# Optimization experiments

Measured on AMD Instinct MI355X. Metric: run time of the kernel, lower is better.

Reference implementation:

```python
import jax, jax.numpy as jnp
import numpy as np

B, S, DIM = 2, 2048, 2048
H, KVH, HD = 16, 4, 128
WINDOW = 1024
SCALE = HD ** -0.5


def setup_inputs() -> dict:
    key = jax.random.key(0)
    ks = jax.random.split(key, 8)
    x = jax.random.normal(ks[0], (B, S, DIM), dtype=jnp.float32)
    # rotary tables (seqlen, head_dim//2)
    inv_freq = 1.0 / (10000.0 ** (jnp.arange(0, HD // 2, dtype=jnp.float32) / (HD // 2)))
    t = jnp.arange(S, dtype=jnp.float32)
    freqs = jnp.outer(t, inv_freq)
    cos = jnp.cos(freqs)
    sin = jnp.sin(freqs)
    positions = jnp.arange(S, dtype=jnp.int64) if jax.config.jax_enable_x64 else jnp.arange(S, dtype=jnp.int32)
    # causal sliding-window mask (S, S): allowed iff q-WINDOW < k <= q
    q_idx = jnp.arange(S)[:, None]
    k_idx = jnp.arange(S)[None, :]
    allowed = (k_idx <= q_idx) & (k_idx > q_idx - WINDOW)
    mask = jnp.where(allowed, 0.0, -1e9).astype(jnp.float32)
    wq = jax.random.normal(ks[1], (DIM, H * HD), dtype=jnp.float32) * (DIM ** -0.5)
    wk = jax.random.normal(ks[2], (DIM, KVH * HD), dtype=jnp.float32) * (DIM ** -0.5)
    wv = jax.random.normal(ks[3], (DIM, KVH * HD), dtype=jnp.float32) * (DIM ** -0.5)
    wo = jax.random.normal(ks[4], (H * HD, DIM), dtype=jnp.float32) * ((H * HD) ** -0.5)
    return {"x": x, "cos": cos, "sin": sin, "positions": positions, "mask": mask,
            "wq": wq, "wk": wk, "wv": wv, "wo": wo}


def _rope(q, k, cos, sin):
    # q,k: (B,S,heads,HD); cos,sin: (S, HD//2)
    half = q.shape[-1] // 2
    qr, qi = q[..., :half], q[..., half:]
    kr, ki = k[..., :half], k[..., half:]
    c = cos[None, :, None, :]
    s = sin[None, :, None, :]
    qc, qs = qr * c, qr * s
    kc, ks_ = kr * c, kr * s
    # faithful to source: out has 1.5*HD features (rotated real half + raw imag half)
    q_out = jnp.concatenate([qc - qs, qc + qs, qi], axis=-1)
    k_out = jnp.concatenate([kc - ks_, kc + ks_, ki], axis=-1)
    return q_out, k_out


def reference(x, cos, sin, positions, mask, wq, wk, wv, wo):
    b, s, _ = x.shape
    xq = (x @ wq).reshape(b, s, H, HD)
    xk = (x @ wk).reshape(b, s, KVH, HD)
    xv = (x @ wv).reshape(b, s, KVH, HD)
    xq, xk = _rope(xq, xk, cos, sin)  # (b,s,H,1.5*HD), (b,s,KVH,1.5*HD)
    repeats = H // KVH
    key = jnp.repeat(xk, repeats, axis=2)   # (b,s,H,1.5*HD)
    value = jnp.repeat(xv, repeats, axis=2)  # (b,s,H,HD)
    scores = jnp.einsum('bqhe,bkhe->bhqk', xq, key) * SCALE
    scores = scores + mask[None, None, :, :]
    probs = jax.nn.softmax(scores.astype(jnp.float32), axis=-1).astype(xq.dtype)
    out = jnp.einsum('bhqk,bkhd->bqhd', probs, value)
    out = out.reshape(b, s, H * HD)
    return out @ wo
```

## Files before the change

kernel.cpp:

```cpp
#include <hip/hip_runtime.h>


typedef __attribute__((ext_vector_type(4))) float f32x4;
typedef __attribute__((ext_vector_type(8))) short s16x8;
typedef __attribute__((ext_vector_type(4))) unsigned short u16x4;

#define DEV static __device__ __forceinline__

DEV unsigned short f2bf(float f) {
  unsigned int u = __float_as_uint(f);
  u += 0x7fffu + ((u >> 16) & 1u);
  return (unsigned short)(u >> 16);
}
DEV float bf2f(unsigned short us) {
  return __uint_as_float(((unsigned int)us) << 16);
}
DEV f32x4 mfma_bf16(s16x8 a, s16x8 b, f32x4 c) {
  return __builtin_amdgcn_mfma_f32_16x16x32_bf16(a, b, c, 0, 0, 0);
}

__global__ void k_sentinel(float* __restrict__ out, int n) {
  int i = blockIdx.x * blockDim.x + threadIdx.x;
  const int stride = gridDim.x * blockDim.x;
  for (; i < n; i += stride) out[i] = 1.0e6f;
}

__global__ void k_cvt_x(const float* __restrict__ x, unsigned short* __restrict__ xb, int n4) {
  int i = blockIdx.x * blockDim.x + threadIdx.x;
  const int stride = gridDim.x * blockDim.x;
  for (; i < n4; i += stride) {
    float4 v = ((const float4*)x)[i];
    u16x4 o = {f2bf(v.x), f2bf(v.y), f2bf(v.z), f2bf(v.w)};
    ((u16x4*)xb)[i] = o;
  }
}

__global__ void k_cvt_w(const float* __restrict__ w, unsigned short* __restrict__ wt,
                        int N, int qscale) {
  __shared__ unsigned short tile[64][66];
  const int n0 = blockIdx.x * 64, k0 = blockIdx.y * 64;
  const int t = threadIdx.x;
  const float SC = 0.08838834764831845f;
#pragma unroll
  for (int i = 0; i < 16; ++i) {
    const int idx = i * 256 + t;
    const int r = idx >> 6, c = idx & 63;
    float v = w[(k0 + r) * N + n0 + c];
    if (qscale) v *= ((((n0 + c) & 127) < 64) ? 2.f * SC : SC);
    tile[r][c] = f2bf(v);
  }
  __syncthreads();
#pragma unroll
  for (int i = 0; i < 16; ++i) {
    const int idx = i * 256 + t;
    const int rn = idx >> 6, ck = idx & 63;
    wt[(n0 + rn) * 2048 + k0 + ck] = tile[ck][rn];
  }
}

__global__ __launch_bounds__(256) void k_gemm(
    const unsigned short* __restrict__ A, const unsigned short* __restrict__ B,
    const int mode, unsigned short* __restrict__ Qo, unsigned short* __restrict__ Kp,
    unsigned short* __restrict__ Vo, float* __restrict__ Co,
    const float* __restrict__ cosp, const float* __restrict__ sinp) {
  __shared__ __align__(16) unsigned short As[4096];
  __shared__ __align__(16) unsigned short Bs[4096];
  char* As_c = (char*)As;
  char* Bs_c = (char*)Bs;
  const int t = threadIdx.x;
  const int lane = t & 63, wid = t >> 6;
  const int l16 = lane & 15, g = lane >> 4;
  const int wr = wid >> 1, wc = wid & 1;
  const int m0 = blockIdx.x * 128, n0 = blockIdx.y * 128;

  const unsigned short* pa = A + (m0 + (t >> 2)) * 2048 + ((t & 3) << 3);
  const unsigned short* pb = B + (n0 + (t >> 2)) * 2048 + ((t & 3) << 3);
  char* la = As_c + t * 16;
  char* lb = Bs_c + t * 16;

  f32x4 acc[4][4] = {};

  for (int kt = 0; kt < 64; ++kt) {
    const unsigned short* pak = pa + kt * 32;
    const unsigned short* pbk = pb + kt * 32;
    s16x8 a0 = *(const s16x8*)(pak);
    s16x8 a1 = *(const s16x8*)(pak + 64 * 2048);
    s16x8 b0 = *(const s16x8*)(pbk);
    s16x8 b1 = *(const s16x8*)(pbk + 64 * 2048);
    __syncthreads();
    *(s16x8*)la = a0;
    *(s16x8*)(la + 4096) = a1;
    *(s16x8*)lb = b0;
    *(s16x8*)(lb + 4096) = b1;
    __syncthreads();
    s16x8 af[4], bfr[4];
#pragma unroll
    for (int i = 0; i < 4; ++i) {
      af[i]  = *(const s16x8*)(As_c + (wr * 64 + i * 16 + l16) * 64 + g * 16);
      bfr[i] = *(const s16x8*)(Bs_c + (wc * 64 + i * 16 + l16) * 64 + g * 16);
    }
#pragma unroll
    for (int i = 0; i < 4; ++i)
#pragma unroll
      for (int j = 0; j < 4; ++j) acc[i][j] = mfma_bf16(af[i], bfr[j], acc[i][j]);
  }

#pragma unroll
  for (int i = 0; i < 4; ++i) {
#pragma unroll
    for (int j = 0; j < 4; ++j) {
#pragma unroll
      for (int r = 0; r < 4; ++r) {
        const float val = acc[i][j][r];
        const int m = m0 + wr * 64 + i * 16 + g * 4 + r;
        const int n = n0 + wc * 64 + j * 16 + l16;
        if (mode == 2) {
          Co[m * 2048 + n] = val;
        } else {
          const int bb = m >> 11, s = m & 2047;
          if (mode == 0) {
            const int hh = n >> 7, d = n & 127;
            Qo[((bb * 16 + hh) * 2048 + s) * 128 + d] = f2bf(val);
          } else if (n < 512) {
            const int kv = n >> 7, d = n & 127;
            unsigned short* kr = Kp + ((bb * 4 + kv) * 2048 + s) * 192;
            if (d < 64) {
              const float c = cosp[s * 64 + d], sn = sinp[s * 64 + d];
              kr[d]      = f2bf(val * c);
              kr[64 + d] = f2bf(val * sn);
            } else {
              kr[64 + d] = f2bf(val);
            }
          } else {
            const int n2 = n - 512, kv = n2 >> 7, d = n2 & 127;
            Vo[((bb * 4 + kv) * 128 + d) * 2048 + s] = f2bf(val);
          }
        }
      }
    }
  }
}

__global__ __launch_bounds__(256) void k_attn(
    const unsigned short* __restrict__ Qb, const unsigned short* __restrict__ Kpb,
    const unsigned short* __restrict__ VTb, const float* __restrict__ cosp,
    const float* __restrict__ sinp, unsigned short* __restrict__ Ob) {
  __shared__ __align__(16) char Ks[24576];
  __shared__ __align__(16) char Vs[16384];
  __shared__ __align__(16) unsigned short Ps[4][1024];
  const int t = threadIdx.x;
  const int wid = t >> 6, lane = t & 63;
  const int l = lane & 15, g = lane >> 4;
  const int qt = blockIdx.x, h = blockIdx.y, b = blockIdx.z;
  const int kvh = h >> 2;
  const int w0 = qt * 64 + wid * 16;

  const unsigned short* qptr = Qb + ((b * 16 + h) * 2048 + (w0 + l)) * 128;
  s16x8 q0 = *(const s16x8*)(qptr + g * 8);
  s16x8 q1 = *(const s16x8*)(qptr + 32 + g * 8);
  s16x8 qf6[6];
  {
    const float* cr = cosp + (w0 + l) * 64 + g * 8;
    const float* sr = sinp + (w0 + l) * 64 + g * 8;
#pragma unroll
    for (int j = 0; j < 8; ++j) {
      const float v0 = bf2f((unsigned short)q0[j]);
      const float v1 = bf2f((unsigned short)q1[j]);
      qf6[0][j] = (short)f2bf(v0 * cr[j]);
      qf6[1][j] = (short)f2bf(v1 * cr[32 + j]);
      qf6[2][j] = (short)f2bf(v0 * sr[j]);
      qf6[3][j] = (short)f2bf(v1 * sr[32 + j]);
    }
  }
  qf6[4] = *(const s16x8*)(qptr + 64 + g * 8);
  qf6[5] = *(const s16x8*)(qptr + 96 + g * 8);

  f32x4 O[8] = {};
  float mrow[4] = {-1e30f, -1e30f, -1e30f, -1e30f};
  float lrow[4] = {0.f, 0.f, 0.f, 0.f};

  const unsigned short* kbase = Kpb + (b * 4 + kvh) * (2048 * 192);
  const unsigned short* vbase = VTb + (b * 4 + kvh) * (128 * 2048);

  int kb0 = qt * 64 - 1023;
  if (kb0 < 0) kb0 = 0;
  kb0 &= ~63;
  const int kbend = qt * 64;

  const int krow = t >> 2, kq = t & 3;

  for (int kb = kb0; kb <= kbend; kb += 64) {
    __syncthreads();
    {
      const unsigned short* ksrc = kbase + (kb + krow) * 192 + kq * 8;
      char* kdst = Ks + krow * 384;
      const int sw = (krow & 7) << 4;
#pragma unroll
      for (int j = 0; j < 6; ++j) {
        s16x8 v = *(const s16x8*)(ksrc + 32 * j);
        *(s16x8*)(kdst + ((kq * 16 + 64 * j) ^ sw)) = v;
      }
    }
#pragma unroll
    for (int p = 0; p < 4; ++p) {
      const int o = (p * 256 + t) * 16;
      const int d = o >> 7, cb = o & 127;
      s16x8 v = *(const s16x8*)(vbase + d * 2048 + kb + (cb >> 1));
      *(s16x8*)(Vs + d * 128 + (cb ^ ((d & 7) << 4))) = v;
    }
    __syncthreads();
    if (kb + 63 < w0 - 1023 || kb > w0 + 15) continue;
    const bool interior = (kb >= w0 - 1008) && (kb + 63 <= w0);

    f32x4 sc[4];
#pragma unroll
    for (int hf = 0; hf < 4; ++hf) {
      f32x4 acc = {0.f, 0.f, 0.f, 0.f};
      const int key = hf * 16 + l;
      const char* kr = Ks + key * 384;
      const int sw = (key & 7) << 4;
#pragma unroll
      for (int c = 0; c < 6; ++c) {
        s16x8 kf = *(const s16x8*)(kr + ((c * 64 + g * 16) ^ sw));
        acc = mfma_bf16(qf6[c], kf, acc);
      }
      sc[hf] = acc;
    }

#pragma unroll
    for (int r = 0; r < 4; ++r) {
      const int q = w0 + g * 4 + r;
      float s0 = sc[0][r], s1 = sc[1][r], s2 = sc[2][r], s3 = sc[3][r];
      if (!interior) {
        const int kg = kb + l;
        if (kg      > q || kg      <= q - 1024) s0 = -1e30f;
        if (kg + 16 > q || kg + 16 <= q - 1024) s1 = -1e30f;
        if (kg + 32 > q || kg + 32 <= q - 1024) s2 = -1e30f;
        if (kg + 48 > q || kg + 48 <= q - 1024) s3 = -1e30f;
      }
      float mx = fmaxf(fmaxf(s0, s1), fmaxf(s2, s3));
      mx = fmaxf(mx, __shfl_xor(mx, 1));
      mx = fmaxf(mx, __shfl_xor(mx, 2));
      mx = fmaxf(mx, __shfl_xor(mx, 4));
      mx = fmaxf(mx, __shfl_xor(mx, 8));
      const float mn = fmaxf(mrow[r], mx);
      const float al = __expf(mrow[r] - mn);
      const float p0 = __expf(s0 - mn), p1 = __expf(s1 - mn);
      const float p2 = __expf(s2 - mn), p3 = __expf(s3 - mn);
      float rs = (p0 + p1) + (p2 + p3);
      rs += __shfl_xor(rs, 1);
      rs += __shfl_xor(rs, 2);
      rs += __shfl_xor(rs, 4);
      rs += __shfl_xor(rs, 8);
      lrow[r] = lrow[r] * al + rs;
      mrow[r] = mn;
#pragma unroll
      for (int d2 = 0; d2 < 8; ++d2) O[d2][r] *= al;
      unsigned short* prow = &Ps[wid][(g * 4 + r) * 64];
      prow[l]      = f2bf(p0);
      prow[l + 16] = f2bf(p1);
      prow[l + 32] = f2bf(p2);
      prow[l + 48] = f2bf(p3);
    }

    const s16x8 pf0 = *(const s16x8*)(&Ps[wid][l * 64 + g * 8]);
    const s16x8 pf1 = *(const s16x8*)(&Ps[wid][l * 64 + 32 + g * 8]);
#pragma unroll
    for (int d2 = 0; d2 < 8; ++d2) {
      const int d = d2 * 16 + l;
      const int sw = (d & 7) << 4;
      s16x8 vf0 = *(const s16x8*)(Vs + d * 128 + ((g * 16) ^ sw));
      s16x8 vf1 = *(const s16x8*)(Vs + d * 128 + ((64 + g * 16) ^ sw));
      O[d2] = mfma_bf16(pf0, vf0, O[d2]);
      O[d2] = mfma_bf16(pf1, vf1, O[d2]);
    }
  }

#pragma unroll
  for (int r = 0; r < 4; ++r) {
    const float inv = 1.0f / lrow[r];
    const int m = b * 2048 + w0 + g * 4 + r;
    unsigned short* orow = Ob + m * 2048 + h * 128;
#pragma unroll
    for (int d2 = 0; d2 < 8; ++d2) orow[d2 * 16 + l] = f2bf(O[d2][r] * inv);
  }
}

extern "C" void kernel_launch(void* const* d_in, const int* in_sizes, int n_in,
                              void* d_out, int out_size, void* d_ws, size_t ws_size,
                              hipStream_t stream) {
  (void)in_sizes; (void)n_in; (void)out_size;
  const float* x    = (const float*)d_in[0];
  const float* cosp = (const float*)d_in[1];
  const float* sinp = (const float*)d_in[2];
  const float* wq = (const float*)d_in[5];
  const float* wk = (const float*)d_in[6];
  const float* wv = (const float*)d_in[7];
  const float* wo = (const float*)d_in[8];
  float* out = (float*)d_out;

  if (ws_size < 25165824u) {
    k_sentinel<<<2048, 256, 0, stream>>>(out, 8388608);
    return;
  }

  char* ws = (char*)d_ws;
  unsigned short* xb  = (unsigned short*)(ws);
  unsigned short* wsl = (unsigned short*)(ws + 16777216);

  char* oc = (char*)d_out;
  unsigned short* Qb  = (unsigned short*)(oc);
  unsigned short* Kp  = (unsigned short*)(oc + 16777216);
  unsigned short* VTb = (unsigned short*)(oc + 23068672);

  k_cvt_x<<<2048, 256, 0, stream>>>(x, xb, 2097152);
  k_cvt_w<<<dim3(32, 32), 256, 0, stream>>>(wq, wsl, 2048, 1);
  k_gemm<<<dim3(32, 16), 256, 0, stream>>>(xb, wsl, 0, Qb, Kp, VTb, nullptr,
                                           cosp, sinp);
  k_cvt_w<<<dim3(8, 32), 256, 0, stream>>>(wk, wsl, 512, 0);
  k_cvt_w<<<dim3(8, 32), 256, 0, stream>>>(wv, wsl + 1048576, 512, 0);
  k_gemm<<<dim3(32, 8), 256, 0, stream>>>(xb, wsl, 1, Qb, Kp, VTb, nullptr,
                                          cosp, sinp);
  k_cvt_w<<<dim3(32, 32), 256, 0, stream>>>(wo, wsl, 2048, 0);
  k_attn<<<dim3(32, 16, 2), 256, 0, stream>>>(Qb, Kp, VTb, cosp, sinp, xb);
  k_gemm<<<dim3(32, 16), 256, 0, stream>>>(xb, wsl, 2, nullptr, nullptr, nullptr,
                                           out, nullptr, nullptr);
}
```

Baseline: 482.7 us.

## Rewrite attention with 32x32 MFMA, 128-query tiles and register-prefetched K/V

The attention kernel now uses 32x32x16 bf16 MFMA. Each block covers 128 queries instead of 64, so every K/V tile loaded into LDS serves twice as many queries. Scores are computed transposed (K times Q), so the probabilities sit in registers already laid out as MFMA operands, and the per-wave LDS P round trip is gone. The next K/V tile is loaded into registers while the current tile computes, which overlaps global loads with math. In exchange the kernel holds more registers (launch bounds set to 2 blocks) and launches half as many blocks, so there is less parallelism and some extra masked tiles at the window edges.

```diff
diff --git a/kernel.cpp b/kernel.cpp
--- a/kernel.cpp
+++ b/kernel.cpp
@@ -2,7 +2,9 @@
 
 
 typedef __attribute__((ext_vector_type(4))) float f32x4;
+typedef __attribute__((ext_vector_type(16))) float f32x16;
 typedef __attribute__((ext_vector_type(8))) short s16x8;
+typedef __attribute__((ext_vector_type(4))) short s16x4;
 typedef __attribute__((ext_vector_type(4))) unsigned short u16x4;
 
 #define DEV static __device__ __forceinline__
@@ -17,6 +19,9 @@
 }
 DEV f32x4 mfma_bf16(s16x8 a, s16x8 b, f32x4 c) {
   return __builtin_amdgcn_mfma_f32_16x16x32_bf16(a, b, c, 0, 0, 0);
+}
+DEV f32x16 mfma32(s16x8 a, s16x8 b, f32x16 c) {
+  return __builtin_amdgcn_mfma_f32_32x32x16_bf16(a, b, c, 0, 0, 0);
 }
 
 __global__ void k_sentinel(float* __restrict__ out, int n) {
@@ -141,148 +146,172 @@
   }
 }
 
-__global__ __launch_bounds__(256) void k_attn(
+__global__ __launch_bounds__(256, 2) void k_attn(
     const unsigned short* __restrict__ Qb, const unsigned short* __restrict__ Kpb,
     const unsigned short* __restrict__ VTb, const float* __restrict__ cosp,
     const float* __restrict__ sinp, unsigned short* __restrict__ Ob) {
   __shared__ __align__(16) char Ks[24576];
   __shared__ __align__(16) char Vs[16384];
-  __shared__ __align__(16) unsigned short Ps[4][1024];
   const int t = threadIdx.x;
   const int wid = t >> 6, lane = t & 63;
-  const int l = lane & 15, g = lane >> 4;
+  const int l5 = lane & 31, g2 = lane >> 5;
   const int qt = blockIdx.x, h = blockIdx.y, b = blockIdx.z;
   const int kvh = h >> 2;
-  const int w0 = qt * 64 + wid * 16;
-
-  const unsigned short* qptr = Qb + ((b * 16 + h) * 2048 + (w0 + l)) * 128;
-  s16x8 q0 = *(const s16x8*)(qptr + g * 8);
-  s16x8 q1 = *(const s16x8*)(qptr + 32 + g * 8);
-  s16x8 qf6[6];
-  {
-    const float* cr = cosp + (w0 + l) * 64 + g * 8;
-    const float* sr = sinp + (w0 + l) * 64 + g * 8;
+  const int qb0 = qt * 128;
+  const int w0 = qb0 + wid * 32;
+  const int qrow = w0 + l5;
+
+  const unsigned short* qp = Qb + ((b * 16 + h) * 2048 + qrow) * 128;
+  const float* crow_ = cosp + qrow * 64;
+  const float* srow_ = sinp + qrow * 64;
+  s16x8 qf[12];
+#pragma unroll
+  for (int ec = 0; ec < 4; ++ec) {
+    const int i0 = ec * 16 + g2 * 8;
+    s16x8 qr = *(const s16x8*)(qp + i0);
+    s16x8 fc, fs;
 #pragma unroll
     for (int j = 0; j < 8; ++j) {
-      const float v0 = bf2f((unsigned short)q0[j]);
-      const float v1 = bf2f((unsigned short)q1[j]);
-      qf6[0][j] = (short)f2bf(v0 * cr[j]);
-      qf6[1][j] = (short)f2bf(v1 * cr[32 + j]);
-      qf6[2][j] = (short)f2bf(v0 * sr[j]);
-      qf6[3][j] = (short)f2bf(v1 * sr[32 + j]);
-    }
-  }
-  qf6[4] = *(const s16x8*)(qptr + 64 + g * 8);
-  qf6[5] = *(const s16x8*)(qptr + 96 + g * 8);
-
-  f32x4 O[8] = {};
-  float mrow[4] = {-1e30f, -1e30f, -1e30f, -1e30f};
-  float lrow[4] = {0.f, 0.f, 0.f, 0.f};
+      const float v = bf2f((unsigned short)qr[j]);
+      fc[j] = (short)f2bf(v * crow_[i0 + j]);
+      fs[j] = (short)f2bf(v * srow_[i0 + j]);
+    }
+    qf[ec] = fc;
+    qf[ec + 4] = fs;
+    qf[ec + 8] = *(const s16x8*)(qp + 64 + i0);
+  }
+
+  f32x16 O[4] = {};
+  float m_r = -1e30f, l_r = 0.f;
 
   const unsigned short* kbase = Kpb + (b * 4 + kvh) * (2048 * 192);
   const unsigned short* vbase = VTb + (b * 4 + kvh) * (128 * 2048);
 
-  int kb0 = qt * 64 - 1023;
+  int kb0 = qb0 - 1023;
   if (kb0 < 0) kb0 = 0;
   kb0 &= ~63;
-  const int kbend = qt * 64;
+  const int kbend = qb0 + 64;
+  const int nt = ((kbend - kb0) >> 6) + 1;
 
   const int krow = t >> 2, kq = t & 3;
-
-  for (int kb = kb0; kb <= kbend; kb += 64) {
+  s16x8 kpre[6], vpre[4];
+
+#define LOADK(KB)                                                              \
+  {                                                                            \
+    const unsigned short* ksrc = kbase + ((KB) + krow) * 192 + kq * 8;         \
+    _Pragma("unroll") for (int j = 0; j < 6; ++j)                              \
+        kpre[j] = *(const s16x8*)(ksrc + 32 * j);                              \
+    _Pragma("unroll") for (int p = 0; p < 4; ++p) {                            \
+      const int o = (p * 256 + t) * 16;                                        \
+      vpre[p] = *(const s16x8*)(vbase + (o >> 7) * 2048 + (KB) + ((o & 127) >> 1)); \
+    }                                                                          \
+  }
+#define WRITEK()                                                               \
+  {                                                                            \
+    char* kdst = Ks + krow * 384;                                              \
+    const int swk = (krow & 7) << 4;                                           \
+    _Pragma("unroll") for (int j = 0; j < 6; ++j)                              \
+        *(s16x8*)(kdst + ((kq * 16 + 64 * j) ^ swk)) = kpre[j];                \
+    _Pragma("unroll") for (int p = 0; p < 4; ++p) {                            \
+      const int o = (p * 256 + t) * 16;                                        \
+      const int d = o >> 7, cb = o & 127;                                      \
+      *(s16x8*)(Vs + d * 128 + (cb ^ ((d & 7) << 4))) = vpre[p];               \
+    }                                                                          \
+  }
+
+  LOADK(kb0);
+  WRITEK();
+  __syncthreads();
+
+  for (int it = 0; it < nt; ++it) {
+    const int kb = kb0 + (it << 6);
+    const bool havenext = (it + 1 < nt);
+    if (havenext) LOADK(kb + 64);
+
+    if (kb + 63 >= w0 - 1023 && kb <= w0 + 31) {
+      const bool interior = (kb >= w0 - 992) && (kb <= w0 - 63);
+
+      f32x16 s0 = {}, s1 = {};
+#pragma unroll
+      for (int ec = 0; ec < 12; ++ec) {
+        const int colb = ec * 32 + g2 * 16;
+        const int r0 = l5, r1 = 32 + l5;
+        s16x8 kf0 = *(const s16x8*)(Ks + r0 * 384 + (colb ^ ((r0 & 7) << 4)));
+        s16x8 kf1 = *(const s16x8*)(Ks + r1 * 384 + (colb ^ ((r1 & 7) << 4)));
+        s0 = mfma32(kf0, qf[ec], s0);
+        s1 = mfma32(kf1, qf[ec], s1);
+      }
+
+      if (!interior) {
+#pragma unroll
+        for (int r = 0; r < 16; ++r) {
+          const int kl = (r & 3) + 8 * (r >> 2) + 4 * g2;
+          const int k0g = kb + kl, k1g = kb + 32 + kl;
+          if (k0g > qrow || k0g <= qrow - 1024) s0[r] = -1e30f;
+          if (k1g > qrow || k1g <= qrow - 1024) s1[r] = -1e30f;
+        }
+      }
+      float mt = -1e30f;
+#pragma unroll
+      for (int r = 0; r < 16; ++r) mt = fmaxf(mt, fmaxf(s0[r], s1[r]));
+      mt = fmaxf(mt, __shfl_xor(mt, 32));
+      const float mn = fmaxf(m_r, mt);
+      const float al = __expf(m_r - mn);
+      m_r = mn;
+      float p0[16], p1[16];
+      float ps = 0.f;
+#pragma unroll
+      for (int r = 0; r < 16; ++r) {
+        p0[r] = __expf(s0[r] - mn);
+        p1[r] = __expf(s1[r] - mn);
+        ps += p0[r] + p1[r];
+      }
+      ps += __shfl_xor(ps, 32);
+      l_r = l_r * al + ps;
+#pragma unroll
+      for (int db = 0; db < 4; ++db) O[db] = O[db] * al;
+
+      s16x8 pf[4];
+#pragma unroll
+      for (int kc = 0; kc < 4; ++kc) {
+#pragma unroll
+        for (int j = 0; j < 8; ++j) {
+          const float pv = (kc < 2) ? p0[8 * (kc & 1) + j] : p1[8 * (kc & 1) + j];
+          pf[kc][j] = (short)f2bf(pv);
+        }
+      }
+
+#pragma unroll
+      for (int db = 0; db < 4; ++db) {
+#pragma unroll
+        for (int kc = 0; kc < 4; ++kc) {
+          const int d = db * 32 + l5;
+          const int swv = (d & 7) << 4;
+          const int c0 = kc * 32 + 8 * g2;
+          s16x4 lo = *(const s16x4*)(Vs + d * 128 + (c0 ^ swv));
+          s16x4 hi = *(const s16x4*)(Vs + d * 128 + ((c0 + 16) ^ swv));
+          s16x8 vf = {lo[0], lo[1], lo[2], lo[3], hi[0], hi[1], hi[2], hi[3]};
+          O[db] = mfma32(vf, pf[kc], O[db]);
+        }
+      }
+    }
+
     __syncthreads();
-    {
-      const unsigned short* ksrc = kbase + (kb + krow) * 192 + kq * 8;
-      char* kdst = Ks + krow * 384;
-      const int sw = (krow & 7) << 4;
-#pragma unroll
-      for (int j = 0; j < 6; ++j) {
-        s16x8 v = *(const s16x8*)(ksrc + 32 * j);
-        *(s16x8*)(kdst + ((kq * 16 + 64 * j) ^ sw)) = v;
-      }
-    }
-#pragma unroll
-    for (int p = 0; p < 4; ++p) {
-      const int o = (p * 256 + t) * 16;
-      const int d = o >> 7, cb = o & 127;
-      s16x8 v = *(const s16x8*)(vbase + d * 2048 + kb + (cb >> 1));
-      *(s16x8*)(Vs + d * 128 + (cb ^ ((d & 7) << 4))) = v;
-    }
+    if (havenext) WRITEK();
     __syncthreads();
-    if (kb + 63 < w0 - 1023 || kb > w0 + 15) continue;
-    const bool interior = (kb >= w0 - 1008) && (kb + 63 <= w0);
-
-    f32x4 sc[4];
-#pragma unroll
-    for (int hf = 0; hf < 4; ++hf) {
-      f32x4 acc = {0.f, 0.f, 0.f, 0.f};
-      const int key = hf * 16 + l;
-      const char* kr = Ks + key * 384;
-      const int sw = (key & 7) << 4;
-#pragma unroll
-      for (int c = 0; c < 6; ++c) {
-        s16x8 kf = *(const s16x8*)(kr + ((c * 64 + g * 16) ^ sw));
-        acc = mfma_bf16(qf6[c], kf, acc);
-      }
-      sc[hf] = acc;
-    }
-
-#pragma unroll
-    for (int r = 0; r < 4; ++r) {
-      const int q = w0 + g * 4 + r;
-      float s0 = sc[0][r], s1 = sc[1][r], s2 = sc[2][r], s3 = sc[3][r];
-      if (!interior) {
-        const int kg = kb + l;
-        if (kg      > q || kg      <= q - 1024) s0 = -1e30f;
-        if (kg + 16 > q || kg + 16 <= q - 1024) s1 = -1e30f;
-        if (kg + 32 > q || kg + 32 <= q - 1024) s2 = -1e30f;
-        if (kg + 48 > q || kg + 48 <= q - 1024) s3 = -1e30f;
-      }
-      float mx = fmaxf(fmaxf(s0, s1), fmaxf(s2, s3));
-      mx = fmaxf(mx, __shfl_xor(mx, 1));
-      mx = fmaxf(mx, __shfl_xor(mx, 2));
-      mx = fmaxf(mx, __shfl_xor(mx, 4));
-      mx = fmaxf(mx, __shfl_xor(mx, 8));
-      const float mn = fmaxf(mrow[r], mx);
-      const float al = __expf(mrow[r] - mn);
-      const float p0 = __expf(s0 - mn), p1 = __expf(s1 - mn);
-      const float p2 = __expf(s2 - mn), p3 = __expf(s3 - mn);
-      float rs = (p0 + p1) + (p2 + p3);
-      rs += __shfl_xor(rs, 1);
-      rs += __shfl_xor(rs, 2);
-      rs += __shfl_xor(rs, 4);
-      rs += __shfl_xor(rs, 8);
-      lrow[r] = lrow[r] * al + rs;
-      mrow[r] = mn;
-#pragma unroll
-      for (int d2 = 0; d2 < 8; ++d2) O[d2][r] *= al;
-      unsigned short* prow = &Ps[wid][(g * 4 + r) * 64];
-      prow[l]      = f2bf(p0);
-      prow[l + 16] = f2bf(p1);
-      prow[l + 32] = f2bf(p2);
-      prow[l + 48] = f2bf(p3);
-    }
-
-    const s16x8 pf0 = *(const s16x8*)(&Ps[wid][l * 64 + g * 8]);
-    const s16x8 pf1 = *(const s16x8*)(&Ps[wid][l * 64 + 32 + g * 8]);
-#pragma unroll
-    for (int d2 = 0; d2 < 8; ++d2) {
-      const int d = d2 * 16 + l;
-      const int sw = (d & 7) << 4;
-      s16x8 vf0 = *(const s16x8*)(Vs + d * 128 + ((g * 16) ^ sw));
-      s16x8 vf1 = *(const s16x8*)(Vs + d * 128 + ((64 + g * 16) ^ sw));
-      O[d2] = mfma_bf16(pf0, vf0, O[d2]);
-      O[d2] = mfma_bf16(pf1, vf1, O[d2]);
-    }
-  }
-
-#pragma unroll
-  for (int r = 0; r < 4; ++r) {
-    const float inv = 1.0f / lrow[r];
-    const int m = b * 2048 + w0 + g * 4 + r;
-    unsigned short* orow = Ob + m * 2048 + h * 128;
-#pragma unroll
-    for (int d2 = 0; d2 < 8; ++d2) orow[d2 * 16 + l] = f2bf(O[d2][r] * inv);
+  }
+
+  const float linv = 1.0f / l_r;
+  unsigned short* ob = Ob + ((unsigned)(b * 2048 + qrow)) * 2048 + h * 128;
+#pragma unroll
+  for (int db = 0; db < 4; ++db) {
+#pragma unroll
+    for (int r = 0; r < 16; r += 2) {
+      const int d = db * 32 + (r & 3) + 8 * (r >> 2) + 4 * g2;
+      const unsigned int uo = (unsigned int)f2bf(O[db][r] * linv) |
+                              ((unsigned int)f2bf(O[db][r + 1] * linv) << 16);
+      *(unsigned int*)(ob + d) = uo;
+    }
   }
 }
 
@@ -322,7 +351,7 @@
   k_gemm<<<dim3(32, 8), 256, 0, stream>>>(xb, wsl, 1, Qb, Kp, VTb, nullptr,
                                           cosp, sinp);
   k_cvt_w<<<dim3(32, 32), 256, 0, stream>>>(wo, wsl, 2048, 0);
-  k_attn<<<dim3(32, 16, 2), 256, 0, stream>>>(Qb, Kp, VTb, cosp, sinp, xb);
+  k_attn<<<dim3(16, 16, 2), 256, 0, stream>>>(Qb, Kp, VTb, cosp, sinp, xb);
   k_gemm<<<dim3(32, 16), 256, 0, stream>>>(xb, wsl, 2, nullptr, nullptr, nullptr,
                                            out, nullptr, nullptr);
 }
```

New measurement: 409.1 us. 1.18x faster.
